# Kernel optimization log

Hardware: AMD Instinct MI355X
Metric: run time of the kernel (lower is better)

Reference implementation:

```python
import jax, jax.numpy as jnp
import numpy as np

DIM = 1024
NUM_HEADS = 16
HEAD_DIM = DIM // NUM_HEADS
SCALE = HEAD_DIM ** -0.5


def setup_inputs() -> dict:
    key = jax.random.key(0)
    k1, k2, k3 = jax.random.split(key, 3)
    B, N = 2, 2048
    x = jax.random.normal(k1, (B, N, DIM), dtype=jnp.float32)
    W_qkv = jax.random.normal(k2, (DIM, 3 * DIM), dtype=jnp.float32) * (DIM ** -0.5)
    b_qkv = jnp.zeros((3 * DIM,), dtype=jnp.float32)
    W_proj = jax.random.normal(k3, (DIM, DIM), dtype=jnp.float32) * (DIM ** -0.5)
    b_proj = jnp.zeros((DIM,), dtype=jnp.float32)
    return {"x": x, "W_qkv": W_qkv, "b_qkv": b_qkv, "W_proj": W_proj, "b_proj": b_proj}


def reference(x, W_qkv, b_qkv, W_proj, b_proj):
    B, N, D = x.shape
    qkv = x @ W_qkv + b_qkv                      # [B, N, 3D]
    qkv = qkv.reshape(B, N, 3, NUM_HEADS, HEAD_DIM)
    qkv = jnp.transpose(qkv, (2, 0, 3, 1, 4))    # [3, B, H, N, hd]
    q, k, v = qkv[0], qkv[1], qkv[2]
    attn = jnp.einsum('bhqd,bhkd->bhqk', q, k) * SCALE  # [B, H, N, N]
    attn = jax.nn.softmax(attn, axis=-1)
    out = jnp.einsum('bhqk,bhkd->bhqd', attn, v)        # [B, H, N, hd]
    out = jnp.transpose(out, (0, 2, 1, 3)).reshape(B, N, D)
    out = out @ W_proj + b_proj
    return out
```

## Files before the change

kernel.cpp:

```cpp
#include <hip/hip_runtime.h>


typedef __bf16 bf16_t;
typedef __bf16 bf16x2 __attribute__((ext_vector_type(2)));
typedef __bf16 bf16x4 __attribute__((ext_vector_type(4)));
typedef __bf16 bf16x8 __attribute__((ext_vector_type(8)));
typedef float  f32x4  __attribute__((ext_vector_type(4)));

#define NTOK 2048
#define DIM  1024
#define NH   16
#define HD   64
#define SCL2 0.18033688011112042f

#define MFMA16(a, b, c) __builtin_amdgcn_mfma_f32_16x16x32_bf16((a), (b), (c), 0, 0, 0)

__device__ __forceinline__ void gload_lds16(const void* g, void* l) {
  __builtin_amdgcn_global_load_lds((const __attribute__((address_space(1))) void*)g,
                                   (__attribute__((address_space(3))) void*)l, 16, 0, 0);
}

__device__ __forceinline__ void transpose_cvt_tile(const float* __restrict__ W,
                                                   bf16_t* __restrict__ WT,
                                                   int cols, int bx, int by) {
  __shared__ float tile[32][33];
  int j0 = bx * 32, i0 = by * 32;
  int c = threadIdx.x & 31, r0 = threadIdx.x >> 5;
#pragma unroll
  for (int it = 0; it < 4; ++it) {
    int r = r0 + it * 8;
    tile[r][c] = W[(long)(i0 + r) * cols + j0 + c];
  }
  __syncthreads();
#pragma unroll
  for (int it = 0; it < 4; ++it) {
    int r = r0 + it * 8;
    int orow = j0 + r, ocol = i0 + c;
    WT[(long)orow * 1024 + ((((ocol >> 3) ^ (orow & 7)) << 3) | (ocol & 7))] =
        (bf16_t)tile[c][r];
  }
}

__global__ __launch_bounds__(256) void k_prep(const float* __restrict__ x,
                                              bf16_t* __restrict__ xb,
                                              const float* __restrict__ Wq,
                                              bf16_t* __restrict__ WqT,
                                              const float* __restrict__ Wp,
                                              bf16_t* __restrict__ WpT) {
  int id = blockIdx.x;
  if (id < 2048) {
    int i = (id * 256 + threadIdx.x) * 8;
    float4 a = *(const float4*)(x + i);
    float4 b = *(const float4*)(x + i + 4);
    bf16x8 v;
    v[0] = (bf16_t)a.x; v[1] = (bf16_t)a.y; v[2] = (bf16_t)a.z; v[3] = (bf16_t)a.w;
    v[4] = (bf16_t)b.x; v[5] = (bf16_t)b.y; v[6] = (bf16_t)b.z; v[7] = (bf16_t)b.w;
    int r = i >> 10, c = (i & 1023) >> 3;
    *(bf16x8*)(xb + r * 1024 + ((c ^ (r & 7)) << 3)) = v;
  } else if (id < 2048 + 3072) {
    int t = id - 2048;
    transpose_cvt_tile(Wq, WqT, 3072, t % 96, t / 96);
  } else {
    int t = id - 5120;
    transpose_cvt_tile(Wp, WpT, 1024, t & 31, t >> 5);
  }
}

__device__ __forceinline__ void gemm_core(const bf16_t* __restrict__ A,
                                          const bf16_t* __restrict__ B,
                                          int K, int bm, int bn,
                                          bf16_t* As, bf16_t* Bs, f32x4 acc[4][4]) {
  const int t = threadIdx.x;
  const int lane = t & 63;
  const int w = t >> 6;
  const int wr = (w >> 1) * 64, wc = (w & 1) * 64;
  const int l15 = lane & 15, g = lane >> 4;
  const int srow = t >> 3, scol = (t & 7) * 8;
  const f32x4 vzero = {0.f, 0.f, 0.f, 0.f};
#pragma unroll
  for (int m = 0; m < 4; ++m)
#pragma unroll
    for (int n = 0; n < 4; ++n) acc[m][n] = vzero;

  const bf16_t* ga = A + (long)(bm + srow) * K + scol;
  const bf16_t* gb = B + (long)(bn + srow) * K + scol;
  bf16_t* lA = As + srow * 64 + scol;
  bf16_t* lB = Bs + srow * 64 + scol;
  const int xr = l15 & 7;

  for (int k0 = 0; k0 < K; k0 += 64) {
#pragma unroll
    for (int j = 0; j < 4; ++j) {
      gload_lds16(ga + (long)32 * j * K + k0, lA + j * 2048);
      gload_lds16(gb + (long)32 * j * K + k0, lB + j * 2048);
    }
    __syncthreads();
#pragma unroll
    for (int kk = 0; kk < 2; ++kk) {
      bf16x8 af[4], bfv[4];
#pragma unroll
      for (int m = 0; m < 4; ++m)
        af[m] = *(const bf16x8*)((const char*)As + (wr + m * 16 + l15) * 128 +
                                 (((kk * 4 + g) ^ xr) << 4));
#pragma unroll
      for (int n = 0; n < 4; ++n)
        bfv[n] = *(const bf16x8*)((const char*)Bs + (wc + n * 16 + l15) * 128 +
                                  (((kk * 4 + g) ^ xr) << 4));
#pragma unroll
      for (int m = 0; m < 4; ++m)
#pragma unroll
        for (int n = 0; n < 4; ++n)
          acc[m][n] = MFMA16(af[m], bfv[n], acc[m][n]);
    }
    __syncthreads();
  }
}

__global__ __launch_bounds__(256) void k_gemm_qkv(const bf16_t* __restrict__ xb,
                                                  const bf16_t* __restrict__ WqT,
                                                  const float* __restrict__ bq,
                                                  bf16_t* __restrict__ Qb,
                                                  bf16_t* __restrict__ Kb,
                                                  bf16_t* __restrict__ Vt) {
  __shared__ alignas(16) bf16_t As[128 * 64];
  __shared__ alignas(16) bf16_t Bs[128 * 64];
  f32x4 acc[4][4];
  const int bm = blockIdx.y * 128, bn = blockIdx.x * 128;
  gemm_core(xb, WqT, DIM, bm, bn, As, Bs, acc);

  const int lane = threadIdx.x & 63, w = threadIdx.x >> 6;
  const int wr = (w >> 1) * 64, wc = (w & 1) * 64;
  const int l15 = lane & 15, g = lane >> 4;
#pragma unroll
  for (int n = 0; n < 4; ++n) {
    int col = bn + wc + n * 16 + l15;
    float bias = bq[col];
    int t3 = col >> 10, rem = col & 1023;
    int h = rem >> 6, d = rem & 63;
#pragma unroll
    for (int m = 0; m < 4; ++m) {
      int rowb = bm + wr + m * 16 + g * 4;
#pragma unroll
      for (int r = 0; r < 4; ++r) {
        int row = rowb + r;
        int b = row >> 11, tok = row & 2047;
        int bh = b * NH + h;
        float val = acc[m][n][r] + bias;
        if (t3 == 0) {
          Qb[bh * (NTOK * HD) + tok * HD + d] = (bf16_t)(val * SCL2);
        } else if (t3 == 1) {
          int rr = tok & 63;
          int off = bh * (NTOK * HD) + (tok >> 6) * 4096 + rr * 64 +
                    (((d >> 3) ^ (rr & 7)) << 3) + (d & 7);
          Kb[off] = (bf16_t)val;
        } else {
          int ct = tok & 63;
          int off = bh * (NTOK * HD) + (tok >> 6) * 4096 + d * 64 +
                    (((ct >> 3) ^ (d & 7)) << 3) + (ct & 7);
          Vt[off] = (bf16_t)val;
        }
      }
    }
  }
}

__global__ __launch_bounds__(256, 3) void k_attn(const bf16_t* __restrict__ Qb,
                                                 const bf16_t* __restrict__ Kb,
                                                 const bf16_t* __restrict__ Vt,
                                                 bf16_t* __restrict__ Ob) {
  __shared__ alignas(16) bf16_t Ks[2][64 * 64];
  __shared__ alignas(16) bf16_t Vs[2][64 * 64];
  __shared__ alignas(16) char  P2[4][4096];

  const int b0 = blockIdx.x;
  const int swz = (b0 & 7) * 64 + (b0 >> 3);
  const int qt = swz & 15, bh = swz >> 4;
  const int b = bh >> 4, h = bh & 15;
  const int t = threadIdx.x;
  const int w = t >> 6, lane = t & 63;
  const int l15 = lane & 15, g = lane >> 4;
  const bf16_t* Qp = Qb + bh * (NTOK * HD);
  const bf16_t* Kp = Kb + bh * (NTOK * HD);
  const bf16_t* Vp = Vt + bh * (NTOK * HD);
  const int q0 = qt * 128 + w * 32;
  char* P2w = &P2[w][0];

  const int cs0 = ((g ^ (l15 & 7)) << 4);
  const int cs1 = cs0 ^ 64;

  bf16x8 qfr[2][2];
#pragma unroll
  for (int qf = 0; qf < 2; ++qf)
#pragma unroll
    for (int kk = 0; kk < 2; ++kk)
      qfr[qf][kk] = *(const bf16x8*)(Qp + (q0 + qf * 16 + l15) * HD + kk * 32 + g * 8);

  bf16x8 ones;
#pragma unroll
  for (int i = 0; i < 8; ++i) ones[i] = (bf16_t)1.0f;

  const f32x4 vzero = {0.f, 0.f, 0.f, 0.f};
  f32x4 o[2][4];
#pragma unroll
  for (int qf = 0; qf < 2; ++qf)
#pragma unroll
    for (int df = 0; df < 4; ++df) o[qf][df] = vzero;
  f32x4 o_sum[2] = {vzero, vzero};

  auto stage = [&](int buf, int tile) {
    const bf16_t* gk = Kp + tile * 4096 + t * 8;
    const bf16_t* gv = Vp + tile * 4096 + t * 8;
    gload_lds16(gk,        (char*)Ks[buf] + t * 16);
    gload_lds16(gk + 2048, (char*)Ks[buf] + 4096 + t * 16);
    gload_lds16(gv,        (char*)Vs[buf] + t * 16);
    gload_lds16(gv + 2048, (char*)Vs[buf] + 4096 + t * 16);
  };

  stage(0, 0);
  __syncthreads();
  int cur = 0;

  for (int kt = 0; kt < NTOK; kt += 64) {
    if (kt + 64 < NTOK) stage(cur ^ 1, (kt >> 6) + 1);
    const char* kbuf = (const char*)Ks[cur];
    const char* vbuf = (const char*)Vs[cur];
    f32x4 s[2][4];
    __builtin_amdgcn_s_setprio(1);
#pragma unroll
    for (int kf = 0; kf < 4; ++kf) {
      int rb = (kf * 16 + l15) * 128;
      bf16x8 ka0 = *(const bf16x8*)(kbuf + rb + cs0);
      bf16x8 ka1 = *(const bf16x8*)(kbuf + rb + cs1);
      s[0][kf] = MFMA16(ka0, qfr[0][0], vzero);
      s[1][kf] = MFMA16(ka0, qfr[1][0], vzero);
      s[0][kf] = MFMA16(ka1, qfr[0][1], s[0][kf]);
      s[1][kf] = MFMA16(ka1, qfr[1][1], s[1][kf]);
    }
    __builtin_amdgcn_s_setprio(0);
#pragma unroll
    for (int qf = 0; qf < 2; ++qf)
#pragma unroll
      for (int kf = 0; kf < 4; ++kf) {
        bf16x4 pw;
        pw[0] = (bf16_t)__builtin_amdgcn_exp2f(s[qf][kf][0]);
        pw[1] = (bf16_t)__builtin_amdgcn_exp2f(s[qf][kf][1]);
        pw[2] = (bf16_t)__builtin_amdgcn_exp2f(s[qf][kf][2]);
        pw[3] = (bf16_t)__builtin_amdgcn_exp2f(s[qf][kf][3]);
        *(bf16x4*)(P2w + qf * 2048 + (2 * kf + (g >> 1)) * 256 + l15 * 16 + 8 * (g & 1)) = pw;
      }
    __builtin_amdgcn_s_setprio(1);
#pragma unroll
    for (int kb = 0; kb < 2; ++kb) {
      bf16x8 pf0 = *(const bf16x8*)(P2w + kb * 1024 + lane * 16);
      bf16x8 pf1 = *(const bf16x8*)(P2w + 2048 + kb * 1024 + lane * 16);
      int csk = kb ? cs1 : cs0;
      o_sum[0] = MFMA16(ones, pf0, o_sum[0]);
      o_sum[1] = MFMA16(ones, pf1, o_sum[1]);
#pragma unroll
      for (int df = 0; df < 4; ++df) {
        bf16x8 va = *(const bf16x8*)(vbuf + (df * 16 + l15) * 128 + csk);
        o[0][df] = MFMA16(va, pf0, o[0][df]);
        o[1][df] = MFMA16(va, pf1, o[1][df]);
      }
    }
    __builtin_amdgcn_s_setprio(0);
    __syncthreads();
    cur ^= 1;
  }
#pragma unroll
  for (int qf = 0; qf < 2; ++qf) {
    float inv = 1.0f / o_sum[qf][0];
    int tok = q0 + qf * 16 + l15;
    bf16_t* oprow = Ob + (long)(b * NTOK + tok) * DIM;
    const int xr = l15 & 7;
#pragma unroll
    for (int df = 0; df < 4; ++df) {
#pragma unroll
      for (int rp = 0; rp < 2; ++rp) {
        bf16x2 v2;
        v2[0] = (bf16_t)(o[qf][df][rp * 2]     * inv);
        v2[1] = (bf16_t)(o[qf][df][rp * 2 + 1] * inv);
        int c = h * 8 + df * 2 + (g >> 1);
        *(bf16x2*)(oprow + ((c ^ xr) << 3) + (g & 1) * 4 + rp * 2) = v2;
      }
    }
  }
}

__global__ __launch_bounds__(256) void k_gemm_proj(const bf16_t* __restrict__ Ob,
                                                   const bf16_t* __restrict__ WpT,
                                                   const float* __restrict__ bp,
                                                   float* __restrict__ out) {
  __shared__ alignas(16) bf16_t As[128 * 64];
  __shared__ alignas(16) bf16_t Bs[128 * 64];
  f32x4 acc[4][4];
  const int bm = blockIdx.y * 128, bn = blockIdx.x * 128;
  gemm_core(Ob, WpT, DIM, bm, bn, As, Bs, acc);

  const int lane = threadIdx.x & 63, w = threadIdx.x >> 6;
  const int wr = (w >> 1) * 64, wc = (w & 1) * 64;
  const int l15 = lane & 15, g = lane >> 4;
#pragma unroll
  for (int n = 0; n < 4; ++n) {
    int col = bn + wc + n * 16 + l15;
    float bias = bp[col];
#pragma unroll
    for (int m = 0; m < 4; ++m) {
      int rowb = bm + wr + m * 16 + g * 4;
#pragma unroll
      for (int r = 0; r < 4; ++r)
        out[(long)(rowb + r) * DIM + col] = acc[m][n][r] + bias;
    }
  }
}

extern "C" void kernel_launch(void* const* d_in, const int* in_sizes, int n_in,
                              void* d_out, int out_size, void* d_ws, size_t ws_size,
                              hipStream_t stream) {
  const float* x     = (const float*)d_in[0];
  const float* Wqkv  = (const float*)d_in[1];
  const float* bqkv  = (const float*)d_in[2];
  const float* Wproj = (const float*)d_in[3];
  const float* bproj = (const float*)d_in[4];
  float* out = (float*)d_out;

  char* ws = (char*)d_ws;
  bf16_t* xb  = (bf16_t*)(ws);
  bf16_t* WqT = (bf16_t*)(ws + (8l  << 20));
  bf16_t* WpT = (bf16_t*)(ws + (14l << 20));
  bf16_t* Qb  = (bf16_t*)(ws + (16l << 20));
  bf16_t* Kb  = (bf16_t*)(ws + (24l << 20));
  bf16_t* Vt  = (bf16_t*)(ws + (32l << 20));
  bf16_t* Ob  = (bf16_t*)(ws);

  k_prep<<<6144, 256, 0, stream>>>(x, xb, Wqkv, WqT, Wproj, WpT);
  k_gemm_qkv<<<dim3(24, 32), 256, 0, stream>>>(xb, WqT, bqkv, Qb, Kb, Vt);
  k_attn<<<512, 256, 0, stream>>>(Qb, Kb, Vt, Ob);
  k_gemm_proj<<<dim3(8, 32), 256, 0, stream>>>(Ob, WpT, bproj, out);
}
```

Before: 121.0 us.

## Double-buffer GEMM LDS tiles and remap blocks for XCD-local L2 reuse

The shared GEMM core now uses two LDS buffers, prefetching the next K-tile with global_load_lds while MFMAs run on the current one. This hides global-load latency and drops one barrier per iteration. The QKV and projection GEMMs also switch to a 1D grid, with block indices remapped so that blocks landing on the same XCD share B-columns, aiming for better L2 reuse. LDS per block doubles to 64KB, which may lower occupancy.

```diff
diff --git a/kernel.cpp b/kernel.cpp
--- a/kernel.cpp
+++ b/kernel.cpp
@@ -88,23 +88,32 @@
   bf16_t* lB = Bs + srow * 64 + scol;
   const int xr = l15 & 7;
 
+  auto stageAB = [&](int buf, int k0) {
+#pragma unroll
+    for (int j = 0; j < 4; ++j) {
+      gload_lds16(ga + (long)32 * j * K + k0, lA + buf * 8192 + j * 2048);
+      gload_lds16(gb + (long)32 * j * K + k0, lB + buf * 8192 + j * 2048);
+    }
+  };
+
+  stageAB(0, 0);
+  __syncthreads();
+  int cur = 0;
+
   for (int k0 = 0; k0 < K; k0 += 64) {
-#pragma unroll
-    for (int j = 0; j < 4; ++j) {
-      gload_lds16(ga + (long)32 * j * K + k0, lA + j * 2048);
-      gload_lds16(gb + (long)32 * j * K + k0, lB + j * 2048);
-    }
-    __syncthreads();
+    if (k0 + 64 < K) stageAB(cur ^ 1, k0 + 64);
+    const char* Ab = (const char*)(As + cur * 8192);
+    const char* Bb = (const char*)(Bs + cur * 8192);
 #pragma unroll
     for (int kk = 0; kk < 2; ++kk) {
       bf16x8 af[4], bfv[4];
 #pragma unroll
       for (int m = 0; m < 4; ++m)
-        af[m] = *(const bf16x8*)((const char*)As + (wr + m * 16 + l15) * 128 +
+        af[m] = *(const bf16x8*)(Ab + (wr + m * 16 + l15) * 128 +
                                  (((kk * 4 + g) ^ xr) << 4));
 #pragma unroll
       for (int n = 0; n < 4; ++n)
-        bfv[n] = *(const bf16x8*)((const char*)Bs + (wc + n * 16 + l15) * 128 +
+        bfv[n] = *(const bf16x8*)(Bb + (wc + n * 16 + l15) * 128 +
                                   (((kk * 4 + g) ^ xr) << 4));
 #pragma unroll
       for (int m = 0; m < 4; ++m)
@@ -113,6 +122,7 @@
           acc[m][n] = MFMA16(af[m], bfv[n], acc[m][n]);
     }
     __syncthreads();
+    cur ^= 1;
   }
 }
 
@@ -122,10 +132,13 @@
                                                   bf16_t* __restrict__ Qb,
                                                   bf16_t* __restrict__ Kb,
                                                   bf16_t* __restrict__ Vt) {
-  __shared__ alignas(16) bf16_t As[128 * 64];
-  __shared__ alignas(16) bf16_t Bs[128 * 64];
+  __shared__ alignas(16) bf16_t As[2 * 128 * 64];
+  __shared__ alignas(16) bf16_t Bs[2 * 128 * 64];
   f32x4 acc[4][4];
-  const int bm = blockIdx.y * 128, bn = blockIdx.x * 128;
+  const int bid = blockIdx.x;
+  const int xcd = bid & 7, ib = bid >> 3;
+  const int bn = (xcd * 3 + (ib >> 5)) * 128;
+  const int bm = (ib & 31) * 128;
   gemm_core(xb, WqT, DIM, bm, bn, As, Bs, acc);
 
   const int lane = threadIdx.x & 63, w = threadIdx.x >> 6;
@@ -291,10 +304,12 @@
                                                    const bf16_t* __restrict__ WpT,
                                                    const float* __restrict__ bp,
                                                    float* __restrict__ out) {
-  __shared__ alignas(16) bf16_t As[128 * 64];
-  __shared__ alignas(16) bf16_t Bs[128 * 64];
+  __shared__ alignas(16) bf16_t As[2 * 128 * 64];
+  __shared__ alignas(16) bf16_t Bs[2 * 128 * 64];
   f32x4 acc[4][4];
-  const int bm = blockIdx.y * 128, bn = blockIdx.x * 128;
+  const int bid = blockIdx.x;
+  const int bn = (bid & 7) * 128;
+  const int bm = (bid >> 3) * 128;
   gemm_core(Ob, WpT, DIM, bm, bn, As, Bs, acc);
 
   const int lane = threadIdx.x & 63, w = threadIdx.x >> 6;
@@ -334,7 +349,7 @@
   bf16_t* Ob  = (bf16_t*)(ws);
 
   k_prep<<<6144, 256, 0, stream>>>(x, xb, Wqkv, WqT, Wproj, WpT);
-  k_gemm_qkv<<<dim3(24, 32), 256, 0, stream>>>(xb, WqT, bqkv, Qb, Kb, Vt);
+  k_gemm_qkv<<<768, 256, 0, stream>>>(xb, WqT, bqkv, Qb, Kb, Vt);
   k_attn<<<512, 256, 0, stream>>>(Qb, Kb, Vt, Ob);
-  k_gemm_proj<<<dim3(8, 32), 256, 0, stream>>>(Ob, WpT, bproj, out);
-}
+  k_gemm_proj<<<256, 256, 0, stream>>>(Ob, WpT, bproj, out);
+}
```

After: 119.5 us. About the same (-1.3%).
